# Performance work log

Measured on AMD Instinct MI355X. Metric: run time of the kernel, lower is better.

Reference implementation:

```python
import jax, jax.numpy as jnp
import numpy as np
from jax import lax

D = 64
EPS = 1e-8


def zc_rmsnorm(x, g):
    x0 = x - jnp.mean(x, axis=-1, keepdims=True)
    return x0 * jax.lax.rsqrt(jnp.mean(x0 * x0, axis=-1, keepdims=True) + EPS) * g


def l2norm(x):
    return x * jax.lax.rsqrt(jnp.sum(x * x, axis=-1, keepdims=True) + EPS)


def linear(x, w, b):
    # w: [out, in] (torch layout), x: [..., in]
    return jnp.einsum('btd,od->bto', x, w) + b


def dwconv3(x, w, b):
    # x: [B, T, D]; w: [D, 1, 3] depthwise kernel; padding=1 (SAME)
    xT = jnp.transpose(x, (0, 2, 1))  # [B, D, T]
    y = lax.conv_general_dilated(
        xT, w, window_strides=(1,), padding=[(1, 1)],
        dimension_numbers=('NCH', 'OIH', 'NCH'), feature_group_count=D)
    y = y + b[None, :, None]
    return jnp.transpose(y, (0, 2, 1))  # [B, T, D]


def setup_inputs() -> dict:
    key = jax.random.key(0)
    ks = jax.random.split(key, 24)
    s = 1.0 / np.sqrt(D)
    def lin_wb(k1, k2):
        return (jax.random.uniform(k1, (D, D), jnp.float32, -s, s),
                jax.random.uniform(k2, (D,), jnp.float32, -s, s))
    def conv_wb(k1, k2):
        cs = 1.0 / np.sqrt(3.0)
        return (jax.random.uniform(k1, (D, 1, 3), jnp.float32, -cs, cs),
                jax.random.uniform(k2, (D,), jnp.float32, -cs, cs))
    x = jax.random.normal(ks[0], (64, 4096, D), jnp.float32)
    qw, qb = lin_wb(ks[1], ks[2]); kw, kb = lin_wb(ks[3], ks[4]); vw, vb = lin_wb(ks[5], ks[6])
    qcw, qcb = conv_wb(ks[7], ks[8]); kcw, kcb = conv_wb(ks[9], ks[10]); vcw, vcb = conv_wb(ks[11], ks[12])
    aw, ab = lin_wb(ks[13], ks[14]); bw, bb = lin_wb(ks[15], ks[16])
    pw, pb = lin_wb(ks[17], ks[18])
    return dict(x=x, norm_g=jnp.ones((D,), jnp.float32),
                qw=qw, qb=qb, kw=kw, kb=kb, vw=vw, vb=vb,
                qcw=qcw, qcb=qcb, kcw=kcw, kcb=kcb, vcw=vcw, vcb=vcb,
                aw=aw, ab=ab, bw=bw, bb=bb,
                post_norm_g=jnp.ones((D,), jnp.float32), pw=pw, pb=pb)


def reference(x, norm_g, qw, qb, kw, kb, vw, vb, qcw, qcb, kcw, kcb, vcw, vcb,
              aw, ab, bw, bb, post_norm_g, pw, pb):
    h = zc_rmsnorm(x, norm_g)
    q = jax.nn.sigmoid(dwconv3(linear(h, qw, qb), qcw, qcb))
    k = jax.nn.sigmoid(dwconv3(linear(h, kw, kb), kcw, kcb))
    v = jax.nn.sigmoid(dwconv3(linear(h, vw, vb), vcw, vcb))
    q, k = l2norm(q), l2norm(k)
    delta = q * (k * v)
    delta = jnp.tanh(linear(x, aw, ab)) * delta + linear(x, bw, bb)
    dhat = linear(zc_rmsnorm(delta, post_norm_g), pw, pb)
    # dropout in eval mode (identity)
    return x + jax.nn.sigmoid(jax.nn.silu(dhat)) * dhat
```

## Files before the change

kernel.cpp:

```cpp
#include <hip/hip_runtime.h>


#define TBS 32
#define ROWS 34
#define DD 64
#define T_LEN 4096
#define TILES_PB 128
#define LSTRIDE 72

typedef unsigned short ushort_t;
typedef short bf16x8 __attribute__((ext_vector_type(8)));
typedef float f32x4 __attribute__((ext_vector_type(4)));
typedef float f32x16 __attribute__((ext_vector_type(16)));

__device__ inline float lo2f(unsigned u) { return __uint_as_float(u << 16); }
__device__ inline float hi2f(unsigned u) { return __uint_as_float(u & 0xffff0000u); }
__device__ inline unsigned pk2(float a, float b) {
    unsigned r;
    asm("v_cvt_pk_bf16_f32 %0, %1, %2" : "=v"(r) : "v"(a), "v"(b));
    return r;
}
__device__ inline ushort_t f2b(float f) {
    unsigned u = __float_as_uint(f);
    u += 0x7fffu + ((u >> 16) & 1u);
    return (ushort_t)(u >> 16);
}

__device__ inline float rcp_(float x) {
#if __has_builtin(__builtin_amdgcn_rcpf)
    return __builtin_amdgcn_rcpf(x);
#else
    float r; asm("v_rcp_f32 %0, %1" : "=v"(r) : "v"(x)); return r;
#endif
}
__device__ inline float rsq_(float x) {
#if __has_builtin(__builtin_amdgcn_rsqf)
    return __builtin_amdgcn_rsqf(x);
#else
    float r; asm("v_rsq_f32 %0, %1" : "=v"(r) : "v"(x)); return r;
#endif
}

template<int CTRL>
__device__ inline float dpp_add(float v) {
    int t = __builtin_amdgcn_mov_dpp(__float_as_int(v), CTRL, 0xf, 0xf, true);
    return v + __int_as_float(t);
}
__device__ inline float sum16(float v) {
    v = dpp_add<0x128>(v);
    v = dpp_add<0x124>(v);
    v = dpp_add<0x122>(v);
    v = dpp_add<0x121>(v);
    return v;
}

__device__ inline float sigmoidf_(float x) { return rcp_(1.f + __expf(-x)); }
__device__ inline float tanhf_(float x) {
    float xc = fminf(fmaxf(x, -15.f), 15.f);
    float e2 = __expf(2.f * xc);
    return (e2 - 1.f) * rcp_(e2 + 1.f);
}

__global__ __launch_bounds__(256) void cvt_kernel(
    const float* __restrict__ w0, const float* __restrict__ w1,
    const float* __restrict__ w2, const float* __restrict__ w3,
    const float* __restrict__ w4, const float* __restrict__ w5,
    ushort_t* __restrict__ dst) {
    int i = blockIdx.x * 256 + threadIdx.x;
    const float* ws_[6] = {w0, w1, w2, w3, w4, w5};
    dst[i] = f2b(ws_[i >> 12][i & 4095]);
}

__device__ inline void mm32(const ushort_t* __restrict__ W,
                            const float* __restrict__ bias,
                            const ushort_t* src, ushort_t* dst,
                            int m0, int strip, int lane) {
    const int l31  = lane & 31;
    const int half = lane >> 5;
    const int t    = m0 + l31;
    const ushort_t* wrow = W + (strip * 32 + l31) * 64 + half * 8;
    const ushort_t* arow = src + t * LSTRIDE + half * 8;
    f32x16 acc = {};
#pragma unroll
    for (int kk = 0; kk < 4; kk++) {
        bf16x8 af = *(const bf16x8*)(wrow + kk * 16);
        bf16x8 bf = *(const bf16x8*)(arow + kk * 16);
        acc = __builtin_amdgcn_mfma_f32_32x32x16_bf16(af, bf, acc, 0, 0, 0);
    }
#pragma unroll
    for (int rg = 0; rg < 4; rg++) {
        const int o0 = strip * 32 + rg * 8 + half * 4;
        f32x4 bv = *(const f32x4*)(bias + o0);
        uint2 w;
        w.x = pk2(acc[rg * 4 + 0] + bv[0], acc[rg * 4 + 1] + bv[1]);
        w.y = pk2(acc[rg * 4 + 2] + bv[2], acc[rg * 4 + 3] + bv[3]);
        *(uint2*)(dst + t * LSTRIDE + o0) = w;
    }
}

__device__ inline void conv_sig4(const float* __restrict__ CW,
                                 const float* __restrict__ CB, int cb,
                                 const ushort_t* F, int rr, bool zl, bool zr,
                                 float out[4]) {
    uint2 m_ = *(const uint2*)(F + (rr - 1) * LSTRIDE + cb);
    uint2 c_ = *(const uint2*)(F + rr * LSTRIDE + cb);
    uint2 p_ = *(const uint2*)(F + (rr + 1) * LSTRIDE + cb);
    f32x4 w0 = *(const f32x4*)(CW + cb);
    f32x4 w1 = *(const f32x4*)(CW + 64 + cb);
    f32x4 w2 = *(const f32x4*)(CW + 128 + cb);
    f32x4 bb = *(const f32x4*)(CB + cb);
    float xm[4] = {lo2f(m_.x), hi2f(m_.x), lo2f(m_.y), hi2f(m_.y)};
    float x0[4] = {lo2f(c_.x), hi2f(c_.x), lo2f(c_.y), hi2f(c_.y)};
    float xp[4] = {lo2f(p_.x), hi2f(p_.x), lo2f(p_.y), hi2f(p_.y)};
#pragma unroll
    for (int i = 0; i < 4; i++) {
        float a = fmaf(w0[i], zl ? 0.f : xm[i],
                  fmaf(w1[i], x0[i],
                  fmaf(w2[i], zr ? 0.f : xp[i], bb[i])));
        out[i] = sigmoidf_(a);
    }
}

__global__ __launch_bounds__(512, 8) void gdn_kernel(
    const float* __restrict__ xg, const float* __restrict__ norm_g,
    const ushort_t* __restrict__ wpack,
    const float* __restrict__ qcw, const float* __restrict__ qcb,
    const float* __restrict__ kcw, const float* __restrict__ kcb,
    const float* __restrict__ vcw, const float* __restrict__ vcb,
    const float* __restrict__ qbf, const float* __restrict__ kbf,
    const float* __restrict__ vbf, const float* __restrict__ abf,
    const float* __restrict__ bbf, const float* __restrict__ pbf,
    const float* __restrict__ post_g,
    float* __restrict__ outg, int tiles_per_b) {
    __shared__ __align__(16) ushort_t Xs[ROWS * LSTRIDE];
    __shared__ __align__(16) ushort_t Hs[ROWS * LSTRIDE];
    __shared__ __align__(16) ushort_t Fq[ROWS * LSTRIDE];
    __shared__ __align__(16) ushort_t Fk[ROWS * LSTRIDE];
    __shared__ __align__(16) ushort_t Fv[ROWS * LSTRIDE];
    __shared__ __align__(16) ushort_t Fa[ROWS * LSTRIDE];
    __shared__ __align__(16) ushort_t Fb[ROWS * LSTRIDE];
    __shared__ __align__(16) float CWs[768];

    const int tid    = threadIdx.x;
    const int wave   = tid >> 6;
    const int lane   = tid & 63;
    const int cb     = (tid & 15) * 4;
    const int rgrp   = tid >> 4;
    const int bidx = blockIdx.x;
    const int b    = bidx >> 7;
    const int tile = bidx & (TILES_PB - 1);
    const int t0   = tile * TBS;
    const bool left_edge  = (t0 == 0);
    const bool right_edge = (t0 + TBS >= T_LEN);

    {
        const f32x4 gv = *(const f32x4*)(norm_g + cb);
        for (int r = rgrp; r < ROWS; r += 32) {
            int t = t0 + r - 1;
            f32x4 xv = {0.f, 0.f, 0.f, 0.f};
            if (t >= 0 && t < T_LEN)
                xv = *(const f32x4*)(xg + ((size_t)b * T_LEN + t) * DD + cb);
            float s  = (xv[0] + xv[1]) + (xv[2] + xv[3]);
            float s2 = 0.f;
#pragma unroll
            for (int i = 0; i < 4; i++) s2 = fmaf(xv[i], xv[i], s2);
            s = sum16(s); s2 = sum16(s2);
            float mean = s * (1.f / 64.f);
            float var  = fmaxf(fmaf(-mean, mean, s2 * (1.f / 64.f)), 0.f);
            float inv  = rsq_(var + 1e-8f);
            uint2 xpk; xpk.x = pk2(xv[0], xv[1]); xpk.y = pk2(xv[2], xv[3]);
            *(uint2*)(Xs + r * LSTRIDE + cb) = xpk;
            uint2 hpk;
            hpk.x = pk2((xv[0] - mean) * inv * gv[0], (xv[1] - mean) * inv * gv[1]);
            hpk.y = pk2((xv[2] - mean) * inv * gv[2], (xv[3] - mean) * inv * gv[3]);
            *(uint2*)(Hs + r * LSTRIDE + cb) = hpk;
        }
    }
    if (tid < 192) {
        int tap = tid >> 6, c = tid & 63;
        CWs[tid]       = qcw[c * 3 + tap];
        CWs[192 + tid] = kcw[c * 3 + tap];
        CWs[384 + tid] = vcw[c * 3 + tap];
    } else if (tid < 256) {
        int c = tid - 192;
        CWs[576 + c] = qcb[c];
        CWs[640 + c] = kcb[c];
        CWs[704 + c] = vcb[c];
    }
    __syncthreads();

#pragma unroll
    for (int i = 0; i < 2; i++) {
        const int u = wave * 2 + i;
        const ushort_t* W; const float* bias; const ushort_t* src; ushort_t* dst;
        int m0, strip;
        if (u < 12) {
            const int g = u >> 2, sub = u & 3;
            W = wpack + g * 4096;
            bias = (g == 0) ? qbf : (g == 1) ? kbf : vbf;
            dst  = (g == 0) ? Fq  : (g == 1) ? Fk  : Fv;
            src = Hs;
            m0 = (sub & 2) ? 2 : 0;
            strip = sub & 1;
        } else {
            const int g = (u - 12) >> 1;
            W = wpack + (3 + g) * 4096;
            bias = g ? bbf : abf;
            dst  = g ? Fb  : Fa;
            src = Xs;
            m0 = 1;
            strip = u & 1;
        }
        mm32(W, bias, src, dst, m0, strip, lane);
    }
    __syncthreads();

    {
        const int rr = rgrp + 1;
        const bool zl = (rr == 1) && left_edge;
        const bool zr = (rr == TBS) && right_edge;
        float qs[4], ks[4], vs[4];
        conv_sig4(CWs,       CWs + 576, cb, Fq, rr, zl, zr, qs);
        conv_sig4(CWs + 192, CWs + 640, cb, Fk, rr, zl, zr, ks);
        conv_sig4(CWs + 384, CWs + 704, cb, Fv, rr, zl, zr, vs);
        float sq = 0.f, sk = 0.f;
#pragma unroll
        for (int i = 0; i < 4; i++) {
            sq = fmaf(qs[i], qs[i], sq);
            sk = fmaf(ks[i], ks[i], sk);
        }
        float qi = rsq_(sum16(sq) + 1e-8f);
        float ki = rsq_(sum16(sk) + 1e-8f);
        uint2 av = *(const uint2*)(Fa + rr * LSTRIDE + cb);
        uint2 bv = *(const uint2*)(Fb + rr * LSTRIDE + cb);
        float af[4] = {lo2f(av.x), hi2f(av.x), lo2f(av.y), hi2f(av.y)};
        float bf[4] = {lo2f(bv.x), hi2f(bv.x), lo2f(bv.y), hi2f(bv.y)};
        float d2[4]; float sm = 0.f, sm2 = 0.f;
#pragma unroll
        for (int i = 0; i < 4; i++) {
            float delta = (qs[i] * qi) * (ks[i] * ki) * vs[i];
            d2[i] = fmaf(tanhf_(af[i]), delta, bf[i]);
            sm += d2[i];
            sm2 = fmaf(d2[i], d2[i], sm2);
        }
        sm = sum16(sm); sm2 = sum16(sm2);
        float mean = sm * (1.f / 64.f);
        float var  = fmaxf(fmaf(-mean, mean, sm2 * (1.f / 64.f)), 0.f);
        float inv  = rsq_(var + 1e-8f);
        const f32x4 pgv = *(const f32x4*)(post_g + cb);
        uint2 npk;
        npk.x = pk2((d2[0] - mean) * inv * pgv[0], (d2[1] - mean) * inv * pgv[1]);
        npk.y = pk2((d2[2] - mean) * inv * pgv[2], (d2[3] - mean) * inv * pgv[3]);
        *(uint2*)(Hs + rr * LSTRIDE + cb) = npk;
    }
    __syncthreads();

    if (wave < 2)
        mm32(wpack + 5 * 4096, pbf, Hs, Fq, 1, wave, lane);
    __syncthreads();

    {
        const int rr = rgrp + 1;
        const int t = t0 + rgrp;
        uint2 dpk = *(const uint2*)(Fq + rr * LSTRIDE + cb);
        float dh[4] = {lo2f(dpk.x), hi2f(dpk.x), lo2f(dpk.y), hi2f(dpk.y)};
        const float* xrow = xg + ((size_t)b * T_LEN + t) * DD + cb;
        f32x4 xv = *(const f32x4*)(xrow);
        f32x4 ov;
#pragma unroll
        for (int i = 0; i < 4; i++) {
            float sl = dh[i] * sigmoidf_(dh[i]);
            ov[i] = xv[i] + sigmoidf_(sl) * dh[i];
        }
        *(f32x4*)(outg + ((size_t)b * T_LEN + t) * DD + cb) = ov;
    }
}

extern "C" void kernel_launch(void* const* d_in, const int* in_sizes, int n_in,
                              void* d_out, int out_size, void* d_ws, size_t ws_size,
                              hipStream_t stream) {
    const float* xg     = (const float*)d_in[0];
    const float* norm_g = (const float*)d_in[1];
    const float* qw  = (const float*)d_in[2];
    const float* qb  = (const float*)d_in[3];
    const float* kw  = (const float*)d_in[4];
    const float* kb  = (const float*)d_in[5];
    const float* vw  = (const float*)d_in[6];
    const float* vb  = (const float*)d_in[7];
    const float* qcw = (const float*)d_in[8];
    const float* qcb = (const float*)d_in[9];
    const float* kcw = (const float*)d_in[10];
    const float* kcb = (const float*)d_in[11];
    const float* vcw = (const float*)d_in[12];
    const float* vcb = (const float*)d_in[13];
    const float* aw  = (const float*)d_in[14];
    const float* ab  = (const float*)d_in[15];
    const float* bw  = (const float*)d_in[16];
    const float* bb  = (const float*)d_in[17];
    const float* pg  = (const float*)d_in[18];
    const float* pw  = (const float*)d_in[19];
    const float* pb  = (const float*)d_in[20];

    ushort_t* wpack = (ushort_t*)d_ws;

    hipLaunchKernelGGL(cvt_kernel, dim3(96), dim3(256), 0, stream,
                       qw, kw, vw, aw, bw, pw, wpack);

    const int B = in_sizes[0] / (T_LEN * DD);
    const int tiles_per_b = T_LEN / TBS;
    hipLaunchKernelGGL(gdn_kernel, dim3(B * tiles_per_b), dim3(512), 0, stream,
                       xg, norm_g, wpack, qcw, qcb, kcw, kcb, vcw, vcb,
                       qb, kb, vb, ab, bb, pb, pg,
                       (float*)d_out, tiles_per_b);
}
```

Baseline: 234.9 us.

## Halve time tile, fuse output projection epilogue, drop conv-weight staging

Shrinks each block from 32 to 16 timesteps with 256 threads and one packed shared buffer using tighter strides, so more blocks can be resident. The final projection's MFMA epilogue now applies the sigmoid-silu gating and residual add directly and writes output, which removes a barrier and a shared round trip. Depthwise conv weights are now read straight from global memory instead of being staged in shared memory. In exchange, the 32x32 MFMAs now run on only 16 or 18 valid rows (the rest read unrelated shared data and are discarded), so matrix work per output row roughly doubles.

```diff
diff --git a/kernel.cpp b/kernel.cpp
--- a/kernel.cpp
+++ b/kernel.cpp
@@ -1,12 +1,13 @@
 #include <hip/hip_runtime.h>
 
 
-#define TBS 32
-#define ROWS 34
+#define TBS 16
+#define CROWS 18
 #define DD 64
 #define T_LEN 4096
-#define TILES_PB 128
-#define LSTRIDE 72
+#define TILES_PB 256
+#define HSTR 72
+#define FSTR 68
 
 typedef unsigned short ushort_t;
 typedef short bf16x8 __attribute__((ext_vector_type(8)));
@@ -71,15 +72,14 @@
     dst[i] = f2b(ws_[i >> 12][i & 4095]);
 }
 
-__device__ inline void mm32(const ushort_t* __restrict__ W,
-                            const float* __restrict__ bias,
-                            const ushort_t* src, ushort_t* dst,
-                            int m0, int strip, int lane) {
+__device__ inline void mmu(const ushort_t* __restrict__ W,
+                           const float* __restrict__ bias,
+                           const ushort_t* src, ushort_t* dst,
+                           int strip, int tmax, int lane) {
     const int l31  = lane & 31;
     const int half = lane >> 5;
-    const int t    = m0 + l31;
     const ushort_t* wrow = W + (strip * 32 + l31) * 64 + half * 8;
-    const ushort_t* arow = src + t * LSTRIDE + half * 8;
+    const ushort_t* arow = src + l31 * HSTR + half * 8;
     f32x16 acc = {};
 #pragma unroll
     for (int kk = 0; kk < 4; kk++) {
@@ -87,28 +87,70 @@
         bf16x8 bf = *(const bf16x8*)(arow + kk * 16);
         acc = __builtin_amdgcn_mfma_f32_32x32x16_bf16(af, bf, acc, 0, 0, 0);
     }
-#pragma unroll
-    for (int rg = 0; rg < 4; rg++) {
-        const int o0 = strip * 32 + rg * 8 + half * 4;
-        f32x4 bv = *(const f32x4*)(bias + o0);
-        uint2 w;
-        w.x = pk2(acc[rg * 4 + 0] + bv[0], acc[rg * 4 + 1] + bv[1]);
-        w.y = pk2(acc[rg * 4 + 2] + bv[2], acc[rg * 4 + 3] + bv[3]);
-        *(uint2*)(dst + t * LSTRIDE + o0) = w;
-    }
-}
-
-__device__ inline void conv_sig4(const float* __restrict__ CW,
-                                 const float* __restrict__ CB, int cb,
-                                 const ushort_t* F, int rr, bool zl, bool zr,
-                                 float out[4]) {
-    uint2 m_ = *(const uint2*)(F + (rr - 1) * LSTRIDE + cb);
-    uint2 c_ = *(const uint2*)(F + rr * LSTRIDE + cb);
-    uint2 p_ = *(const uint2*)(F + (rr + 1) * LSTRIDE + cb);
-    f32x4 w0 = *(const f32x4*)(CW + cb);
-    f32x4 w1 = *(const f32x4*)(CW + 64 + cb);
-    f32x4 w2 = *(const f32x4*)(CW + 128 + cb);
-    f32x4 bb = *(const f32x4*)(CB + cb);
+    if (l31 < tmax) {
+#pragma unroll
+        for (int rg = 0; rg < 4; rg++) {
+            const int o0 = strip * 32 + rg * 8 + half * 4;
+            f32x4 bv = *(const f32x4*)(bias + o0);
+            uint2 w;
+            w.x = pk2(acc[rg * 4 + 0] + bv[0], acc[rg * 4 + 1] + bv[1]);
+            w.y = pk2(acc[rg * 4 + 2] + bv[2], acc[rg * 4 + 3] + bv[3]);
+            *(uint2*)(dst + l31 * FSTR + o0) = w;
+        }
+    }
+}
+
+__device__ inline void pm_fused(const ushort_t* __restrict__ W,
+                                const float* __restrict__ pbf,
+                                const ushort_t* Ns,
+                                const float* __restrict__ xrow0,
+                                float* __restrict__ orow0,
+                                int strip, int lane) {
+    const int l31  = lane & 31;
+    const int half = lane >> 5;
+    const ushort_t* wrow = W + (strip * 32 + l31) * 64 + half * 8;
+    const ushort_t* arow = Ns + l31 * HSTR + half * 8;
+    f32x16 acc = {};
+#pragma unroll
+    for (int kk = 0; kk < 4; kk++) {
+        bf16x8 af = *(const bf16x8*)(wrow + kk * 16);
+        bf16x8 bf = *(const bf16x8*)(arow + kk * 16);
+        acc = __builtin_amdgcn_mfma_f32_32x32x16_bf16(af, bf, acc, 0, 0, 0);
+    }
+    if (l31 < TBS) {
+        const float* xr = xrow0 + l31 * DD;
+        float* orow = orow0 + l31 * DD;
+#pragma unroll
+        for (int rg = 0; rg < 4; rg++) {
+            const int o0 = strip * 32 + rg * 8 + half * 4;
+            f32x4 pv = *(const f32x4*)(pbf + o0);
+            f32x4 xv = *(const f32x4*)(xr + o0);
+            f32x4 ov;
+#pragma unroll
+            for (int j = 0; j < 4; j++) {
+                float dh = acc[rg * 4 + j] + pv[j];
+                float sl = dh * sigmoidf_(dh);
+                ov[j] = xv[j] + sigmoidf_(sl) * dh;
+            }
+            *(f32x4*)(orow + o0) = ov;
+        }
+    }
+}
+
+__device__ inline void conv_sig4g(const float* __restrict__ cw,
+                                  const float* __restrict__ cbias, int cb,
+                                  const ushort_t* F, int cr, bool zl, bool zr,
+                                  float out[4]) {
+    uint2 m_ = *(const uint2*)(F + (cr - 1) * FSTR + cb);
+    uint2 c_ = *(const uint2*)(F + cr * FSTR + cb);
+    uint2 p_ = *(const uint2*)(F + (cr + 1) * FSTR + cb);
+    f32x4 a0 = *(const f32x4*)(cw + cb * 3);
+    f32x4 a1 = *(const f32x4*)(cw + cb * 3 + 4);
+    f32x4 a2 = *(const f32x4*)(cw + cb * 3 + 8);
+    f32x4 bb = *(const f32x4*)(cbias + cb);
+    const float w0[4] = {a0[0], a0[3], a1[2], a2[1]};
+    const float w1[4] = {a0[1], a1[0], a1[3], a2[2]};
+    const float w2[4] = {a0[2], a1[1], a2[0], a2[3]};
     float xm[4] = {lo2f(m_.x), hi2f(m_.x), lo2f(m_.y), hi2f(m_.y)};
     float x0[4] = {lo2f(c_.x), hi2f(c_.x), lo2f(c_.y), hi2f(c_.y)};
     float xp[4] = {lo2f(p_.x), hi2f(p_.x), lo2f(p_.y), hi2f(p_.y)};
@@ -121,7 +163,7 @@
     }
 }
 
-__global__ __launch_bounds__(512, 8) void gdn_kernel(
+__global__ __launch_bounds__(256, 8) void gdn_kernel(
     const float* __restrict__ xg, const float* __restrict__ norm_g,
     const ushort_t* __restrict__ wpack,
     const float* __restrict__ qcw, const float* __restrict__ qcb,
@@ -131,31 +173,31 @@
     const float* __restrict__ vbf, const float* __restrict__ abf,
     const float* __restrict__ bbf, const float* __restrict__ pbf,
     const float* __restrict__ post_g,
-    float* __restrict__ outg, int tiles_per_b) {
-    __shared__ __align__(16) ushort_t Xs[ROWS * LSTRIDE];
-    __shared__ __align__(16) ushort_t Hs[ROWS * LSTRIDE];
-    __shared__ __align__(16) ushort_t Fq[ROWS * LSTRIDE];
-    __shared__ __align__(16) ushort_t Fk[ROWS * LSTRIDE];
-    __shared__ __align__(16) ushort_t Fv[ROWS * LSTRIDE];
-    __shared__ __align__(16) ushort_t Fa[ROWS * LSTRIDE];
-    __shared__ __align__(16) ushort_t Fb[ROWS * LSTRIDE];
-    __shared__ __align__(16) float CWs[768];
-
-    const int tid    = threadIdx.x;
-    const int wave   = tid >> 6;
-    const int lane   = tid & 63;
-    const int cb     = (tid & 15) * 4;
-    const int rgrp   = tid >> 4;
+    float* __restrict__ outg) {
+    __shared__ __align__(16) ushort_t SMEM[9448];
+    ushort_t* Fq = SMEM;
+    ushort_t* Fk = SMEM + 1224;
+    ushort_t* Fv = SMEM + 2448;
+    ushort_t* Fa = SMEM + 3672;
+    ushort_t* Fb = SMEM + 4760;
+    ushort_t* Hs = SMEM + 5848;
+    ushort_t* Xs = SMEM + 7144;
+
+    const int tid  = threadIdx.x;
+    const int wave = tid >> 6;
+    const int lane = tid & 63;
+    const int cb   = (tid & 15) * 4;
+    const int rgrp = tid >> 4;
     const int bidx = blockIdx.x;
-    const int b    = bidx >> 7;
+    const int b    = bidx >> 8;
     const int tile = bidx & (TILES_PB - 1);
     const int t0   = tile * TBS;
-    const bool left_edge  = (t0 == 0);
-    const bool right_edge = (t0 + TBS >= T_LEN);
+    const bool left_edge  = (tile == 0);
+    const bool right_edge = (tile == TILES_PB - 1);
 
     {
         const f32x4 gv = *(const f32x4*)(norm_g + cb);
-        for (int r = rgrp; r < ROWS; r += 32) {
+        for (int r = rgrp; r < CROWS; r += 16) {
             int t = t0 + r - 1;
             f32x4 xv = {0.f, 0.f, 0.f, 0.f};
             if (t >= 0 && t < T_LEN)
@@ -168,61 +210,43 @@
             float mean = s * (1.f / 64.f);
             float var  = fmaxf(fmaf(-mean, mean, s2 * (1.f / 64.f)), 0.f);
             float inv  = rsq_(var + 1e-8f);
-            uint2 xpk; xpk.x = pk2(xv[0], xv[1]); xpk.y = pk2(xv[2], xv[3]);
-            *(uint2*)(Xs + r * LSTRIDE + cb) = xpk;
             uint2 hpk;
             hpk.x = pk2((xv[0] - mean) * inv * gv[0], (xv[1] - mean) * inv * gv[1]);
             hpk.y = pk2((xv[2] - mean) * inv * gv[2], (xv[3] - mean) * inv * gv[3]);
-            *(uint2*)(Hs + r * LSTRIDE + cb) = hpk;
-        }
-    }
-    if (tid < 192) {
-        int tap = tid >> 6, c = tid & 63;
-        CWs[tid]       = qcw[c * 3 + tap];
-        CWs[192 + tid] = kcw[c * 3 + tap];
-        CWs[384 + tid] = vcw[c * 3 + tap];
-    } else if (tid < 256) {
-        int c = tid - 192;
-        CWs[576 + c] = qcb[c];
-        CWs[640 + c] = kcb[c];
-        CWs[704 + c] = vcb[c];
+            *(uint2*)(Hs + r * HSTR + cb) = hpk;
+            if (r >= 1 && r <= TBS) {
+                uint2 xpk; xpk.x = pk2(xv[0], xv[1]); xpk.y = pk2(xv[2], xv[3]);
+                *(uint2*)(Xs + (r - 1) * HSTR + cb) = xpk;
+            }
+        }
     }
     __syncthreads();
 
-#pragma unroll
-    for (int i = 0; i < 2; i++) {
-        const int u = wave * 2 + i;
-        const ushort_t* W; const float* bias; const ushort_t* src; ushort_t* dst;
-        int m0, strip;
-        if (u < 12) {
-            const int g = u >> 2, sub = u & 3;
-            W = wpack + g * 4096;
-            bias = (g == 0) ? qbf : (g == 1) ? kbf : vbf;
-            dst  = (g == 0) ? Fq  : (g == 1) ? Fk  : Fv;
-            src = Hs;
-            m0 = (sub & 2) ? 2 : 0;
-            strip = sub & 1;
-        } else {
-            const int g = (u - 12) >> 1;
-            W = wpack + (3 + g) * 4096;
-            bias = g ? bbf : abf;
-            dst  = g ? Fb  : Fa;
-            src = Xs;
-            m0 = 1;
-            strip = u & 1;
-        }
-        mm32(W, bias, src, dst, m0, strip, lane);
+    if (wave == 0) {
+        mmu(wpack,        qbf, Hs, Fq, 0, CROWS, lane);
+        mmu(wpack,        qbf, Hs, Fq, 1, CROWS, lane);
+        mmu(wpack + 4096, kbf, Hs, Fk, 0, CROWS, lane);
+    } else if (wave == 1) {
+        mmu(wpack + 4096, kbf, Hs, Fk, 1, CROWS, lane);
+        mmu(wpack + 8192, vbf, Hs, Fv, 0, CROWS, lane);
+        mmu(wpack + 8192, vbf, Hs, Fv, 1, CROWS, lane);
+    } else if (wave == 2) {
+        mmu(wpack + 12288, abf, Xs, Fa, 0, TBS, lane);
+        mmu(wpack + 12288, abf, Xs, Fa, 1, TBS, lane);
+    } else {
+        mmu(wpack + 16384, bbf, Xs, Fb, 0, TBS, lane);
+        mmu(wpack + 16384, bbf, Xs, Fb, 1, TBS, lane);
     }
     __syncthreads();
 
     {
-        const int rr = rgrp + 1;
-        const bool zl = (rr == 1) && left_edge;
-        const bool zr = (rr == TBS) && right_edge;
+        const int cr = rgrp + 1;
+        const bool zl = left_edge  && (rgrp == 0);
+        const bool zr = right_edge && (rgrp == TBS - 1);
         float qs[4], ks[4], vs[4];
-        conv_sig4(CWs,       CWs + 576, cb, Fq, rr, zl, zr, qs);
-        conv_sig4(CWs + 192, CWs + 640, cb, Fk, rr, zl, zr, ks);
-        conv_sig4(CWs + 384, CWs + 704, cb, Fv, rr, zl, zr, vs);
+        conv_sig4g(qcw, qcb, cb, Fq, cr, zl, zr, qs);
+        conv_sig4g(kcw, kcb, cb, Fk, cr, zl, zr, ks);
+        conv_sig4g(vcw, vcb, cb, Fv, cr, zl, zr, vs);
         float sq = 0.f, sk = 0.f;
 #pragma unroll
         for (int i = 0; i < 4; i++) {
@@ -231,8 +255,8 @@
         }
         float qi = rsq_(sum16(sq) + 1e-8f);
         float ki = rsq_(sum16(sk) + 1e-8f);
-        uint2 av = *(const uint2*)(Fa + rr * LSTRIDE + cb);
-        uint2 bv = *(const uint2*)(Fb + rr * LSTRIDE + cb);
+        uint2 av = *(const uint2*)(Fa + rgrp * FSTR + cb);
+        uint2 bv = *(const uint2*)(Fb + rgrp * FSTR + cb);
         float af[4] = {lo2f(av.x), hi2f(av.x), lo2f(av.y), hi2f(av.y)};
         float bf[4] = {lo2f(bv.x), hi2f(bv.x), lo2f(bv.y), hi2f(bv.y)};
         float d2[4]; float sm = 0.f, sm2 = 0.f;
@@ -251,28 +275,14 @@
         uint2 npk;
         npk.x = pk2((d2[0] - mean) * inv * pgv[0], (d2[1] - mean) * inv * pgv[1]);
         npk.y = pk2((d2[2] - mean) * inv * pgv[2], (d2[3] - mean) * inv * pgv[3]);
-        *(uint2*)(Hs + rr * LSTRIDE + cb) = npk;
+        *(uint2*)(Hs + rgrp * HSTR + cb) = npk;
     }
     __syncthreads();
 
-    if (wave < 2)
-        mm32(wpack + 5 * 4096, pbf, Hs, Fq, 1, wave, lane);
-    __syncthreads();
-
-    {
-        const int rr = rgrp + 1;
-        const int t = t0 + rgrp;
-        uint2 dpk = *(const uint2*)(Fq + rr * LSTRIDE + cb);
-        float dh[4] = {lo2f(dpk.x), hi2f(dpk.x), lo2f(dpk.y), hi2f(dpk.y)};
-        const float* xrow = xg + ((size_t)b * T_LEN + t) * DD + cb;
-        f32x4 xv = *(const f32x4*)(xrow);
-        f32x4 ov;
-#pragma unroll
-        for (int i = 0; i < 4; i++) {
-            float sl = dh[i] * sigmoidf_(dh[i]);
-            ov[i] = xv[i] + sigmoidf_(sl) * dh[i];
-        }
-        *(f32x4*)(outg + ((size_t)b * T_LEN + t) * DD + cb) = ov;
+    if (wave >= 2) {
+        const float* xrow0 = xg   + ((size_t)b * T_LEN + t0) * DD;
+        float*       orow0 = outg + ((size_t)b * T_LEN + t0) * DD;
+        pm_fused(wpack + 20480, pbf, Hs, xrow0, orow0, wave - 2, lane);
     }
 }
 
@@ -307,9 +317,8 @@
                        qw, kw, vw, aw, bw, pw, wpack);
 
     const int B = in_sizes[0] / (T_LEN * DD);
-    const int tiles_per_b = T_LEN / TBS;
-    hipLaunchKernelGGL(gdn_kernel, dim3(B * tiles_per_b), dim3(512), 0, stream,
+    hipLaunchKernelGGL(gdn_kernel, dim3(B * TILES_PB), dim3(256), 0, stream,
                        xg, norm_g, wpack, qcw, qcb, kcw, kcb, vcw, vcb,
                        qb, kb, vb, ab, bb, pb, pg,
-                       (float*)d_out, tiles_per_b);
-}
+                       (float*)d_out);
+}
```

Result: slower. 286.1 us (+21.8%).

## Fold depthwise conv taps into QKV linear weights as three-tap MFMA accumulation

Applied to the files above, without the earlier changes.

The depthwise 3-tap conv is folded algebraically into the q/k/v linear layers. The prep kernel builds per-tap scaled weight matrices and edge-adjusted biases, and the main kernel accumulates three shifted MFMA products instead of running a separate conv pass in scalar code. This removes the conv shared-memory reads, the conv weight staging and the redundant halo-row GEMMs, and shrinks the LDS tiles to 32 rows. The cost is three times the MFMA work per q/k/v tile and rounding each conv-scaled weight product to bf16.

```diff
diff --git a/kernel.cpp b/kernel.cpp
--- a/kernel.cpp
+++ b/kernel.cpp
@@ -62,24 +62,83 @@
 }
 
 __global__ __launch_bounds__(256) void cvt_kernel(
-    const float* __restrict__ w0, const float* __restrict__ w1,
-    const float* __restrict__ w2, const float* __restrict__ w3,
-    const float* __restrict__ w4, const float* __restrict__ w5,
-    ushort_t* __restrict__ dst) {
+    const float* __restrict__ qw, const float* __restrict__ kw,
+    const float* __restrict__ vw, const float* __restrict__ aw,
+    const float* __restrict__ bw, const float* __restrict__ pw,
+    const float* __restrict__ qcw, const float* __restrict__ kcw,
+    const float* __restrict__ vcw,
+    const float* __restrict__ qb, const float* __restrict__ kb,
+    const float* __restrict__ vb,
+    const float* __restrict__ qcb, const float* __restrict__ kcb,
+    const float* __restrict__ vcb,
+    ushort_t* __restrict__ dst, float* __restrict__ bias_out) {
     int i = blockIdx.x * 256 + threadIdx.x;
-    const float* ws_[6] = {w0, w1, w2, w3, w4, w5};
-    dst[i] = f2b(ws_[i >> 12][i & 4095]);
+    int m = i >> 12;
+    int o = (i & 4095) >> 6, k = i & 63;
+    const float* lw[3] = {qw, kw, vw};
+    const float* cw[3] = {qcw, kcw, vcw};
+    float val;
+    if (m < 9) {
+        int g = m / 3, tap = m % 3;
+        val = cw[g][o * 3 + tap] * lw[g][o * 64 + k];
+    } else {
+        const float* w3[3] = {aw, bw, pw};
+        val = w3[m - 9][o * 64 + k];
+    }
+    dst[i] = f2b(val);
+    if (i < 576) {
+        int g = i / 192, j = i % 192, kind = j >> 6, oo = j & 63;
+        const float* lb[3]  = {qb, kb, vb};
+        const float* cbv[3] = {qcb, kcb, vcb};
+        float c0 = cw[g][oo * 3], c1 = cw[g][oo * 3 + 1], c2 = cw[g][oo * 3 + 2];
+        float s = (kind == 0) ? (c0 + c1 + c2)
+                : (kind == 1) ? (c1 + c2)
+                              : (c0 + c1);
+        bias_out[g * 192 + j] = lb[g][oo] * s + cbv[g][oo];
+    }
+}
+
+__device__ inline void mmqkv(const ushort_t* __restrict__ Wg,
+                             const float* __restrict__ bias_g,
+                             const ushort_t* Hs, ushort_t* dst,
+                             int strip, int lane, bool le, bool re) {
+    const int l31  = lane & 31;
+    const int half = lane >> 5;
+    const ushort_t* arow = Hs + l31 * LSTRIDE + half * 8;
+    f32x16 acc = {};
+#pragma unroll
+    for (int tap = 0; tap < 3; tap++) {
+        const ushort_t* wrow = Wg + tap * 4096 + (strip * 32 + l31) * 64 + half * 8;
+        const ushort_t* ar   = arow + tap * LSTRIDE;
+#pragma unroll
+        for (int kk = 0; kk < 4; kk++) {
+            bf16x8 af = *(const bf16x8*)(wrow + kk * 16);
+            bf16x8 bf = *(const bf16x8*)(ar + kk * 16);
+            acc = __builtin_amdgcn_mfma_f32_32x32x16_bf16(af, bf, acc, 0, 0, 0);
+        }
+    }
+    const float* bp = bias_g;
+    if (le && l31 == 0)  bp = bias_g + 64;
+    if (re && l31 == 31) bp = bias_g + 128;
+#pragma unroll
+    for (int rg = 0; rg < 4; rg++) {
+        const int o0 = strip * 32 + rg * 8 + half * 4;
+        f32x4 bv = *(const f32x4*)(bp + o0);
+        uint2 w;
+        w.x = pk2(acc[rg * 4 + 0] + bv[0], acc[rg * 4 + 1] + bv[1]);
+        w.y = pk2(acc[rg * 4 + 2] + bv[2], acc[rg * 4 + 3] + bv[3]);
+        *(uint2*)(dst + l31 * LSTRIDE + o0) = w;
+    }
 }
 
 __device__ inline void mm32(const ushort_t* __restrict__ W,
                             const float* __restrict__ bias,
-                            const ushort_t* src, ushort_t* dst,
-                            int m0, int strip, int lane) {
+                            const ushort_t* src, int src_r0, ushort_t* dst,
+                            int strip, int lane) {
     const int l31  = lane & 31;
     const int half = lane >> 5;
-    const int t    = m0 + l31;
     const ushort_t* wrow = W + (strip * 32 + l31) * 64 + half * 8;
-    const ushort_t* arow = src + t * LSTRIDE + half * 8;
+    const ushort_t* arow = src + (src_r0 + l31) * LSTRIDE + half * 8;
     f32x16 acc = {};
 #pragma unroll
     for (int kk = 0; kk < 4; kk++) {
@@ -94,52 +153,23 @@
         uint2 w;
         w.x = pk2(acc[rg * 4 + 0] + bv[0], acc[rg * 4 + 1] + bv[1]);
         w.y = pk2(acc[rg * 4 + 2] + bv[2], acc[rg * 4 + 3] + bv[3]);
-        *(uint2*)(dst + t * LSTRIDE + o0) = w;
-    }
-}
-
-__device__ inline void conv_sig4(const float* __restrict__ CW,
-                                 const float* __restrict__ CB, int cb,
-                                 const ushort_t* F, int rr, bool zl, bool zr,
-                                 float out[4]) {
-    uint2 m_ = *(const uint2*)(F + (rr - 1) * LSTRIDE + cb);
-    uint2 c_ = *(const uint2*)(F + rr * LSTRIDE + cb);
-    uint2 p_ = *(const uint2*)(F + (rr + 1) * LSTRIDE + cb);
-    f32x4 w0 = *(const f32x4*)(CW + cb);
-    f32x4 w1 = *(const f32x4*)(CW + 64 + cb);
-    f32x4 w2 = *(const f32x4*)(CW + 128 + cb);
-    f32x4 bb = *(const f32x4*)(CB + cb);
-    float xm[4] = {lo2f(m_.x), hi2f(m_.x), lo2f(m_.y), hi2f(m_.y)};
-    float x0[4] = {lo2f(c_.x), hi2f(c_.x), lo2f(c_.y), hi2f(c_.y)};
-    float xp[4] = {lo2f(p_.x), hi2f(p_.x), lo2f(p_.y), hi2f(p_.y)};
-#pragma unroll
-    for (int i = 0; i < 4; i++) {
-        float a = fmaf(w0[i], zl ? 0.f : xm[i],
-                  fmaf(w1[i], x0[i],
-                  fmaf(w2[i], zr ? 0.f : xp[i], bb[i])));
-        out[i] = sigmoidf_(a);
+        *(uint2*)(dst + l31 * LSTRIDE + o0) = w;
     }
 }
 
 __global__ __launch_bounds__(512, 8) void gdn_kernel(
     const float* __restrict__ xg, const float* __restrict__ norm_g,
-    const ushort_t* __restrict__ wpack,
-    const float* __restrict__ qcw, const float* __restrict__ qcb,
-    const float* __restrict__ kcw, const float* __restrict__ kcb,
-    const float* __restrict__ vcw, const float* __restrict__ vcb,
-    const float* __restrict__ qbf, const float* __restrict__ kbf,
-    const float* __restrict__ vbf, const float* __restrict__ abf,
-    const float* __restrict__ bbf, const float* __restrict__ pbf,
-    const float* __restrict__ post_g,
-    float* __restrict__ outg, int tiles_per_b) {
-    __shared__ __align__(16) ushort_t Xs[ROWS * LSTRIDE];
+    const ushort_t* __restrict__ wpack, const float* __restrict__ wsf,
+    const float* __restrict__ abf, const float* __restrict__ bbf,
+    const float* __restrict__ pbf, const float* __restrict__ post_g,
+    float* __restrict__ outg) {
     __shared__ __align__(16) ushort_t Hs[ROWS * LSTRIDE];
-    __shared__ __align__(16) ushort_t Fq[ROWS * LSTRIDE];
-    __shared__ __align__(16) ushort_t Fk[ROWS * LSTRIDE];
-    __shared__ __align__(16) ushort_t Fv[ROWS * LSTRIDE];
-    __shared__ __align__(16) ushort_t Fa[ROWS * LSTRIDE];
-    __shared__ __align__(16) ushort_t Fb[ROWS * LSTRIDE];
-    __shared__ __align__(16) float CWs[768];
+    __shared__ __align__(16) ushort_t Xs[TBS * LSTRIDE];
+    __shared__ __align__(16) ushort_t Fq[TBS * LSTRIDE];
+    __shared__ __align__(16) ushort_t Fk[TBS * LSTRIDE];
+    __shared__ __align__(16) ushort_t Fv[TBS * LSTRIDE];
+    __shared__ __align__(16) ushort_t Fa[TBS * LSTRIDE];
+    __shared__ __align__(16) ushort_t Fb[TBS * LSTRIDE];
 
     const int tid    = threadIdx.x;
     const int wave   = tid >> 6;
@@ -155,7 +185,7 @@
 
     {
         const f32x4 gv = *(const f32x4*)(norm_g + cb);
-        for (int r = rgrp; r < ROWS; r += 32) {
+        auto do_row = [&](int r) {
             int t = t0 + r - 1;
             f32x4 xv = {0.f, 0.f, 0.f, 0.f};
             if (t >= 0 && t < T_LEN)
@@ -168,71 +198,54 @@
             float mean = s * (1.f / 64.f);
             float var  = fmaxf(fmaf(-mean, mean, s2 * (1.f / 64.f)), 0.f);
             float inv  = rsq_(var + 1e-8f);
-            uint2 xpk; xpk.x = pk2(xv[0], xv[1]); xpk.y = pk2(xv[2], xv[3]);
-            *(uint2*)(Xs + r * LSTRIDE + cb) = xpk;
             uint2 hpk;
             hpk.x = pk2((xv[0] - mean) * inv * gv[0], (xv[1] - mean) * inv * gv[1]);
             hpk.y = pk2((xv[2] - mean) * inv * gv[2], (xv[3] - mean) * inv * gv[3]);
             *(uint2*)(Hs + r * LSTRIDE + cb) = hpk;
-        }
-    }
-    if (tid < 192) {
-        int tap = tid >> 6, c = tid & 63;
-        CWs[tid]       = qcw[c * 3 + tap];
-        CWs[192 + tid] = kcw[c * 3 + tap];
-        CWs[384 + tid] = vcw[c * 3 + tap];
-    } else if (tid < 256) {
-        int c = tid - 192;
-        CWs[576 + c] = qcb[c];
-        CWs[640 + c] = kcb[c];
-        CWs[704 + c] = vcb[c];
+            if (r >= 1 && r <= TBS) {
+                uint2 xpk; xpk.x = pk2(xv[0], xv[1]); xpk.y = pk2(xv[2], xv[3]);
+                *(uint2*)(Xs + (r - 1) * LSTRIDE + cb) = xpk;
+            }
+        };
+        do_row(rgrp);
+        if (rgrp >= 30) do_row(rgrp + 2);
     }
     __syncthreads();
 
-#pragma unroll
-    for (int i = 0; i < 2; i++) {
-        const int u = wave * 2 + i;
-        const ushort_t* W; const float* bias; const ushort_t* src; ushort_t* dst;
-        int m0, strip;
-        if (u < 12) {
-            const int g = u >> 2, sub = u & 3;
-            W = wpack + g * 4096;
-            bias = (g == 0) ? qbf : (g == 1) ? kbf : vbf;
-            dst  = (g == 0) ? Fq  : (g == 1) ? Fk  : Fv;
-            src = Hs;
-            m0 = (sub & 2) ? 2 : 0;
-            strip = sub & 1;
-        } else {
-            const int g = (u - 12) >> 1;
-            W = wpack + (3 + g) * 4096;
-            bias = g ? bbf : abf;
-            dst  = g ? Fb  : Fa;
-            src = Xs;
-            m0 = 1;
-            strip = u & 1;
-        }
-        mm32(W, bias, src, dst, m0, strip, lane);
+    if (wave < 6) {
+        const int g = wave >> 1, s = wave & 1;
+        mmqkv(wpack + g * 3 * 4096, wsf + g * 192, Hs,
+              (g == 0) ? Fq : (g == 1) ? Fk : Fv, s, lane,
+              left_edge, right_edge);
+    } else if (wave == 6) {
+        mm32(wpack + 9 * 4096, abf, Xs, 0, Fa, 0, lane);
+        mm32(wpack + 9 * 4096, abf, Xs, 0, Fa, 1, lane);
+    } else {
+        mm32(wpack + 10 * 4096, bbf, Xs, 0, Fb, 0, lane);
+        mm32(wpack + 10 * 4096, bbf, Xs, 0, Fb, 1, lane);
     }
     __syncthreads();
 
     {
-        const int rr = rgrp + 1;
-        const bool zl = (rr == 1) && left_edge;
-        const bool zr = (rr == TBS) && right_edge;
-        float qs[4], ks[4], vs[4];
-        conv_sig4(CWs,       CWs + 576, cb, Fq, rr, zl, zr, qs);
-        conv_sig4(CWs + 192, CWs + 640, cb, Fk, rr, zl, zr, ks);
-        conv_sig4(CWs + 384, CWs + 704, cb, Fv, rr, zl, zr, vs);
+        uint2 qv_ = *(const uint2*)(Fq + rgrp * LSTRIDE + cb);
+        uint2 kv_ = *(const uint2*)(Fk + rgrp * LSTRIDE + cb);
+        uint2 vv_ = *(const uint2*)(Fv + rgrp * LSTRIDE + cb);
+        float qs[4] = {lo2f(qv_.x), hi2f(qv_.x), lo2f(qv_.y), hi2f(qv_.y)};
+        float ks[4] = {lo2f(kv_.x), hi2f(kv_.x), lo2f(kv_.y), hi2f(kv_.y)};
+        float vs[4] = {lo2f(vv_.x), hi2f(vv_.x), lo2f(vv_.y), hi2f(vv_.y)};
         float sq = 0.f, sk = 0.f;
 #pragma unroll
         for (int i = 0; i < 4; i++) {
+            qs[i] = sigmoidf_(qs[i]);
+            ks[i] = sigmoidf_(ks[i]);
+            vs[i] = sigmoidf_(vs[i]);
             sq = fmaf(qs[i], qs[i], sq);
             sk = fmaf(ks[i], ks[i], sk);
         }
         float qi = rsq_(sum16(sq) + 1e-8f);
         float ki = rsq_(sum16(sk) + 1e-8f);
-        uint2 av = *(const uint2*)(Fa + rr * LSTRIDE + cb);
-        uint2 bv = *(const uint2*)(Fb + rr * LSTRIDE + cb);
+        uint2 av = *(const uint2*)(Fa + rgrp * LSTRIDE + cb);
+        uint2 bv = *(const uint2*)(Fb + rgrp * LSTRIDE + cb);
         float af[4] = {lo2f(av.x), hi2f(av.x), lo2f(av.y), hi2f(av.y)};
         float bf[4] = {lo2f(bv.x), hi2f(bv.x), lo2f(bv.y), hi2f(bv.y)};
         float d2[4]; float sm = 0.f, sm2 = 0.f;
@@ -251,18 +264,17 @@
         uint2 npk;
         npk.x = pk2((d2[0] - mean) * inv * pgv[0], (d2[1] - mean) * inv * pgv[1]);
         npk.y = pk2((d2[2] - mean) * inv * pgv[2], (d2[3] - mean) * inv * pgv[3]);
-        *(uint2*)(Hs + rr * LSTRIDE + cb) = npk;
+        *(uint2*)(Hs + (rgrp + 1) * LSTRIDE + cb) = npk;
     }
     __syncthreads();
 
     if (wave < 2)
-        mm32(wpack + 5 * 4096, pbf, Hs, Fq, 1, wave, lane);
+        mm32(wpack + 11 * 4096, pbf, Hs, 1, Fq, wave, lane);
     __syncthreads();
 
     {
-        const int rr = rgrp + 1;
         const int t = t0 + rgrp;
-        uint2 dpk = *(const uint2*)(Fq + rr * LSTRIDE + cb);
+        uint2 dpk = *(const uint2*)(Fq + rgrp * LSTRIDE + cb);
         float dh[4] = {lo2f(dpk.x), hi2f(dpk.x), lo2f(dpk.y), hi2f(dpk.y)};
         const float* xrow = xg + ((size_t)b * T_LEN + t) * DD + cb;
         f32x4 xv = *(const f32x4*)(xrow);
@@ -302,14 +314,14 @@
     const float* pb  = (const float*)d_in[20];
 
     ushort_t* wpack = (ushort_t*)d_ws;
-
-    hipLaunchKernelGGL(cvt_kernel, dim3(96), dim3(256), 0, stream,
-                       qw, kw, vw, aw, bw, pw, wpack);
+    float*    wsf   = (float*)(wpack + 12 * 4096);
+
+    hipLaunchKernelGGL(cvt_kernel, dim3(192), dim3(256), 0, stream,
+                       qw, kw, vw, aw, bw, pw, qcw, kcw, vcw,
+                       qb, kb, vb, qcb, kcb, vcb, wpack, wsf);
 
     const int B = in_sizes[0] / (T_LEN * DD);
-    const int tiles_per_b = T_LEN / TBS;
-    hipLaunchKernelGGL(gdn_kernel, dim3(B * tiles_per_b), dim3(512), 0, stream,
-                       xg, norm_g, wpack, qcw, qcb, kcw, kcb, vcw, vcb,
-                       qb, kb, vb, ab, bb, pb, pg,
-                       (float*)d_out, tiles_per_b);
-}
+    hipLaunchKernelGGL(gdn_kernel, dim3(B * TILES_PB), dim3(512), 0, stream,
+                       xg, norm_g, wpack, wsf, ab, bb, pb, pg,
+                       (float*)d_out);
+}
```

Result: slower. 255.6 us (+8.8%).

## Double time tile to 64 rows and reassign GEMM work per wave

Applied to the files above, without the earlier changes.

Raises the per-block time tile from 32 to 64 rows, so the two conv halo rows are amortized over more outputs and half as many blocks are launched. The wave-to-GEMM mapping changes so each wave keeps one weight matrix and loops over several 32-row strips, and the elementwise stages loop over two half-tiles per thread. Shared memory per block roughly doubles and launch bounds drop to 4 blocks per CU, which lowers occupancy and latency hiding.

```diff
diff --git a/kernel.cpp b/kernel.cpp
--- a/kernel.cpp
+++ b/kernel.cpp
@@ -1,11 +1,11 @@
 #include <hip/hip_runtime.h>
 
 
-#define TBS 32
-#define ROWS 34
+#define TBS 64
+#define ROWS 66
 #define DD 64
 #define T_LEN 4096
-#define TILES_PB 128
+#define TILES_PB 64
 #define LSTRIDE 72
 
 typedef unsigned short ushort_t;
@@ -121,7 +121,7 @@
     }
 }
 
-__global__ __launch_bounds__(512, 8) void gdn_kernel(
+__global__ __launch_bounds__(512, 4) void gdn_kernel(
     const float* __restrict__ xg, const float* __restrict__ norm_g,
     const ushort_t* __restrict__ wpack,
     const float* __restrict__ qcw, const float* __restrict__ qcb,
@@ -131,7 +131,7 @@
     const float* __restrict__ vbf, const float* __restrict__ abf,
     const float* __restrict__ bbf, const float* __restrict__ pbf,
     const float* __restrict__ post_g,
-    float* __restrict__ outg, int tiles_per_b) {
+    float* __restrict__ outg) {
     __shared__ __align__(16) ushort_t Xs[ROWS * LSTRIDE];
     __shared__ __align__(16) ushort_t Hs[ROWS * LSTRIDE];
     __shared__ __align__(16) ushort_t Fq[ROWS * LSTRIDE];
@@ -147,7 +147,7 @@
     const int cb     = (tid & 15) * 4;
     const int rgrp   = tid >> 4;
     const int bidx = blockIdx.x;
-    const int b    = bidx >> 7;
+    const int b    = bidx >> 6;
     const int tile = bidx & (TILES_PB - 1);
     const int t0   = tile * TBS;
     const bool left_edge  = (t0 == 0);
@@ -155,7 +155,7 @@
 
     {
         const f32x4 gv = *(const f32x4*)(norm_g + cb);
-        for (int r = rgrp; r < ROWS; r += 32) {
+        auto do_row = [&](int r) {
             int t = t0 + r - 1;
             f32x4 xv = {0.f, 0.f, 0.f, 0.f};
             if (t >= 0 && t < T_LEN)
@@ -174,7 +174,10 @@
             hpk.x = pk2((xv[0] - mean) * inv * gv[0], (xv[1] - mean) * inv * gv[1]);
             hpk.y = pk2((xv[2] - mean) * inv * gv[2], (xv[3] - mean) * inv * gv[3]);
             *(uint2*)(Hs + r * LSTRIDE + cb) = hpk;
-        }
+        };
+        do_row(rgrp);
+        do_row(rgrp + 32);
+        if (rgrp == 16 || rgrp == 17) do_row(rgrp + 48);
     }
     if (tid < 192) {
         int tap = tid >> 6, c = tid & 63;
@@ -189,34 +192,26 @@
     }
     __syncthreads();
 
-#pragma unroll
-    for (int i = 0; i < 2; i++) {
-        const int u = wave * 2 + i;
-        const ushort_t* W; const float* bias; const ushort_t* src; ushort_t* dst;
-        int m0, strip;
-        if (u < 12) {
-            const int g = u >> 2, sub = u & 3;
-            W = wpack + g * 4096;
-            bias = (g == 0) ? qbf : (g == 1) ? kbf : vbf;
-            dst  = (g == 0) ? Fq  : (g == 1) ? Fk  : Fv;
-            src = Hs;
-            m0 = (sub & 2) ? 2 : 0;
-            strip = sub & 1;
-        } else {
-            const int g = (u - 12) >> 1;
-            W = wpack + (3 + g) * 4096;
-            bias = g ? bbf : abf;
-            dst  = g ? Fb  : Fa;
-            src = Xs;
-            m0 = 1;
-            strip = u & 1;
-        }
-        mm32(W, bias, src, dst, m0, strip, lane);
+    if (wave < 6) {
+        const int g = wave >> 1, s = wave & 1;
+        const ushort_t* W = wpack + g * 4096;
+        const float* bias = (g == 0) ? qbf : (g == 1) ? kbf : vbf;
+        ushort_t* dst     = (g == 0) ? Fq  : (g == 1) ? Fk  : Fv;
+        mm32(W, bias, Hs, dst, 0,  s, lane);
+        mm32(W, bias, Hs, dst, 32, s, lane);
+        mm32(W, bias, Hs, dst, 34, s, lane);
+    } else {
+        const int s = wave & 1;
+        mm32(wpack + 3 * 4096, abf, Xs, Fa, 1,  s, lane);
+        mm32(wpack + 3 * 4096, abf, Xs, Fa, 33, s, lane);
+        mm32(wpack + 4 * 4096, bbf, Xs, Fb, 1,  s, lane);
+        mm32(wpack + 4 * 4096, bbf, Xs, Fb, 33, s, lane);
     }
     __syncthreads();
 
-    {
-        const int rr = rgrp + 1;
+#pragma unroll
+    for (int half_t = 0; half_t < 2; half_t++) {
+        const int rr = rgrp + 1 + half_t * 32;
         const bool zl = (rr == 1) && left_edge;
         const bool zr = (rr == TBS) && right_edge;
         float qs[4], ks[4], vs[4];
@@ -255,14 +250,15 @@
     }
     __syncthreads();
 
-    if (wave < 2)
-        mm32(wpack + 5 * 4096, pbf, Hs, Fq, 1, wave, lane);
+    if (wave < 4)
+        mm32(wpack + 5 * 4096, pbf, Hs, Fq, (wave & 2) ? 33 : 1, wave & 1, lane);
     __syncthreads();
 
-    {
-        const int rr = rgrp + 1;
-        const int t = t0 + rgrp;
-        uint2 dpk = *(const uint2*)(Fq + rr * LSTRIDE + cb);
+#pragma unroll
+    for (int half_t = 0; half_t < 2; half_t++) {
+        const int tr = rgrp + half_t * 32;
+        const int t  = t0 + tr;
+        uint2 dpk = *(const uint2*)(Fq + (tr + 1) * LSTRIDE + cb);
         float dh[4] = {lo2f(dpk.x), hi2f(dpk.x), lo2f(dpk.y), hi2f(dpk.y)};
         const float* xrow = xg + ((size_t)b * T_LEN + t) * DD + cb;
         f32x4 xv = *(const f32x4*)(xrow);
@@ -307,9 +303,8 @@
                        qw, kw, vw, aw, bw, pw, wpack);
 
     const int B = in_sizes[0] / (T_LEN * DD);
-    const int tiles_per_b = T_LEN / TBS;
-    hipLaunchKernelGGL(gdn_kernel, dim3(B * tiles_per_b), dim3(512), 0, stream,
+    hipLaunchKernelGGL(gdn_kernel, dim3(B * TILES_PB), dim3(512), 0, stream,
                        xg, norm_g, wpack, qcw, qcb, kcw, kcb, vcw, vcb,
                        qb, kb, vb, ab, bb, pb, pg,
-                       (float*)d_out, tiles_per_b);
-}
+                       (float*)d_out);
+}
```

New measurement: 216.8 us. 1.08x faster.
